# Kernel optimization log

Hardware: AMD Instinct MI355X
Metric: run time of the kernel (lower is better)

## Reference

```python
import jax, jax.numpy as jnp
import numpy as np
import math

D_MODEL = 1024
NUM_HEADS = 16
HEAD_DIM = D_MODEL // NUM_HEADS


def setup_inputs() -> dict:
    key = jax.random.key(0)
    ks = jax.random.split(key, 9)
    B, T = 4, 2048
    s = 1.0 / math.sqrt(D_MODEL)
    return {
        "x": jax.random.normal(ks[0], (B, T, D_MODEL), dtype=jnp.float32),
        "Wq": jax.random.normal(ks[1], (D_MODEL, D_MODEL), dtype=jnp.float32) * s,
        "bq": jnp.zeros((D_MODEL,), dtype=jnp.float32),
        "Wk": jax.random.normal(ks[2], (D_MODEL, D_MODEL), dtype=jnp.float32) * s,
        "bk": jnp.zeros((D_MODEL,), dtype=jnp.float32),
        "Wv": jax.random.normal(ks[3], (D_MODEL, D_MODEL), dtype=jnp.float32) * s,
        "bv": jnp.zeros((D_MODEL,), dtype=jnp.float32),
        "Wo": jax.random.normal(ks[4], (D_MODEL, D_MODEL), dtype=jnp.float32) * s,
        "bo": jnp.zeros((D_MODEL,), dtype=jnp.float32),
    }


def reference(x, Wq, bq, Wk, bk, Wv, bv, Wo, bo):
    # x: [B, T, D]. Weights stored as [in, out] (torch Linear weight transposed).
    B, T, D = x.shape
    H, Hd = NUM_HEADS, HEAD_DIM

    def heads(w, b):
        # [B,T,D] -> [B,H,T,Hd]
        return (x @ w + b).reshape(B, T, H, Hd).transpose(0, 2, 1, 3)

    q = heads(Wq, bq)
    k = heads(Wk, bk)
    v = heads(Wv, bv)

    scores = jnp.einsum("bhqd,bhkd->bhqk", q, k) / math.sqrt(Hd)
    attn = jax.nn.softmax(scores, axis=-1)  # dropout is identity in eval mode
    ctx = jnp.einsum("bhqk,bhkd->bhqd", attn, v)
    ctx = ctx.transpose(0, 2, 1, 3).reshape(B, T, D)
    return ctx @ Wo + bo
```

## Files before the change

kernel.cpp:

```cpp
#include <hip/hip_runtime.h>
#include <hip/hip_bf16.h>

#define D_MODEL 1024
#define NHEADS  16
#define HD      64
#define BATCH   4
#define SEQ     2048
#define MROWS   (BATCH*SEQ)

typedef __attribute__((ext_vector_type(8))) short bf16x8;
typedef __attribute__((ext_vector_type(4))) float f32x4;
typedef __attribute__((ext_vector_type(16))) float f32x16;
typedef __attribute__((ext_vector_type(2))) float f32x2;
typedef __attribute__((ext_vector_type(4))) unsigned int u32x4;
typedef __attribute__((ext_vector_type(2))) unsigned int u32x2;
#define MFMA16(a,b,c) __builtin_amdgcn_mfma_f32_16x16x32_bf16(a,b,c,0,0,0)
#define MFMA32(a,b,c) __builtin_amdgcn_mfma_f32_32x32x16_bf16(a,b,c,0,0,0)

__device__ __forceinline__ short f2bf(float f) {
    __hip_bfloat16 h = __float2bfloat16(f);
    return *reinterpret_cast<short*>(&h);
}
__device__ __forceinline__ unsigned cvtpk(float a, float b) {
    unsigned r; asm("v_cvt_pk_bf16_f32 %0, %1, %2" : "=v"(r) : "v"(a), "v"(b)); return r;
}
__device__ __forceinline__ float fexp2(float x) {
    float r; asm("v_exp_f32 %0, %1" : "=v"(r) : "v"(x)); return r;
}
__device__ __forceinline__ f32x2 pkadd(f32x2 a, f32x2 b) {
    f32x2 d; asm("v_pk_add_f32 %0, %1, %2" : "=v"(d) : "v"(a), "v"(b)); return d;
}
#define SH2(V,I) __builtin_shufflevector(V, V, I, (I)+1)

typedef const __attribute__((address_space(1))) unsigned char* gas_t;
typedef __attribute__((address_space(3))) unsigned char* las_t;
#define GLD16(gp, lp) __builtin_amdgcn_global_load_lds((gas_t)(gp), (las_t)(lp), 16, 0, 0)

__global__ __launch_bounds__(256) void prep(
    const float* __restrict__ x,
    const float* __restrict__ Wq, const float* __restrict__ Wk,
    const float* __restrict__ Wv, const float* __restrict__ Wo,
    short* __restrict__ xb,
    short* __restrict__ WqT, short* __restrict__ WkT,
    short* __restrict__ WvT, short* __restrict__ WoT)
{
    __shared__ float tile[64][65];
    const int bid = blockIdx.x;
    const int t = threadIdx.x;
    if (bid < 4096) {
        const size_t i = ((size_t)bid * 256 + t) * 8;
        float4 a = *reinterpret_cast<const float4*>(&x[i]);
        float4 b = *reinterpret_cast<const float4*>(&x[i + 4]);
        bf16x8 v;
        v[0]=f2bf(a.x); v[1]=f2bf(a.y); v[2]=f2bf(a.z); v[3]=f2bf(a.w);
        v[4]=f2bf(b.x); v[5]=f2bf(b.y); v[6]=f2bf(b.z); v[7]=f2bf(b.w);
        *reinterpret_cast<bf16x8*>(&xb[i]) = v;
        return;
    }
    const int tt = bid - 4096;
    const int w = tt >> 8;
    const int tl = tt & 255;
    const int bn = (tl & 15) * 64, bk = (tl >> 4) * 64;
    const float* W = (w==0)?Wq:(w==1)?Wk:(w==2)?Wv:Wo;
    short* out     = (w==0)?WqT:(w==1)?WkT:(w==2)?WvT:WoT;
    const int r = t >> 2, c0 = (t & 3) * 16;
    #pragma unroll
    for (int i = 0; i < 16; i += 4) {
        float4 v = *reinterpret_cast<const float4*>(&W[(size_t)(bk + r) * D_MODEL + bn + c0 + i]);
        tile[r][c0+i] = v.x; tile[r][c0+i+1] = v.y; tile[r][c0+i+2] = v.z; tile[r][c0+i+3] = v.w;
    }
    __syncthreads();
    bf16x8 H0, H1;
    #pragma unroll
    for (int i = 0; i < 8; i++) { H0[i] = f2bf(tile[c0 + i][r]); H1[i] = f2bf(tile[c0 + 8 + i][r]); }
    short* hp = &out[(size_t)(bn + r) * D_MODEL + bk + c0];
    *reinterpret_cast<bf16x8*>(hp) = H0;
    *reinterpret_cast<bf16x8*>(hp + 8) = H1;
}

__global__ __launch_bounds__(256) void gemm_qkv(
    const short* __restrict__ A,
    const short* __restrict__ WqT, const short* __restrict__ WkT, const short* __restrict__ WvT,
    const float* __restrict__ bq, const float* __restrict__ bk, const float* __restrict__ bv,
    short* __restrict__ qo, short* __restrict__ ko, short* __restrict__ vo,
    const float qscale)
{
    __shared__ short As[3][128 * 32];
    __shared__ short Bs[3][128 * 32];
    const int tid = threadIdx.x, wave = tid >> 6, lane = tid & 63;
    const int g = lane >> 4, li = lane & 15;
    const int lin = blockIdx.x + blockIdx.y * 24;
    const int swz = (lin & 7) * 192 + (lin >> 3);
    const int bx = swz % 24, by = swz / 24;
    const int which = bx >> 3;
    const int bm = by * 128, bn = (bx & 7) * 128;
    const int wr = wave >> 1, wc = wave & 1;
    const int lrow = lane >> 2, lcol = (lane & 3) * 8;

    const short* BT = (which == 0) ? WqT : (which == 1) ? WkT : WvT;
    const float* bias = (which == 0) ? bq : (which == 1) ? bk : bv;
    short* out = (which == 0) ? qo : (which == 1) ? ko : vo;
    const float scale = (which == 0) ? qscale : 1.0f;

    f32x4 acc[4][4];
    #pragma unroll
    for (int i = 0; i < 4; i++)
        #pragma unroll
        for (int j = 0; j < 4; j++)
            #pragma unroll
            for (int r = 0; r < 4; r++) acc[i][j][r] = 0.f;

#define STAGEG(KS, BUF) do { \
        const int k0_ = (KS) * 32; \
        _Pragma("unroll") \
        for (int c = 0; c < 2; c++) { \
            const int ch = wave + c * 4; \
            const int row = ch * 16 + lrow; \
            GLD16(&A [(size_t)(bm + row) * D_MODEL + k0_ + lcol], &As[BUF][ch * 512]); \
            GLD16(&BT[(size_t)(bn + row) * D_MODEL + k0_ + lcol], &Bs[BUF][ch * 512]); \
        } \
    } while (0)

    STAGEG(0, 0);
    STAGEG(1, 1);

    const int NSTEP = D_MODEL / 32;
    for (int ks = 0; ks < NSTEP; ks++) {
        const int cur = ks % 3;
        if (ks + 2 < NSTEP) {
            STAGEG(ks + 2, (ks + 2) % 3);
            asm volatile("s_waitcnt vmcnt(8)" ::: "memory");
        } else if (ks + 1 < NSTEP) {
            asm volatile("s_waitcnt vmcnt(4)" ::: "memory");
        } else {
            asm volatile("s_waitcnt vmcnt(0)" ::: "memory");
        }
        __builtin_amdgcn_s_barrier();
        __builtin_amdgcn_sched_barrier(0);

        bf16x8 af[4], bfr[4];
        #pragma unroll
        for (int mi = 0; mi < 4; mi++) af[mi]  = *reinterpret_cast<const bf16x8*>(&As[cur][(wr * 64 + mi * 16 + li) * 32 + g * 8]);
        #pragma unroll
        for (int ni = 0; ni < 4; ni++) bfr[ni] = *reinterpret_cast<const bf16x8*>(&Bs[cur][(wc * 64 + ni * 16 + li) * 32 + g * 8]);
        #pragma unroll
        for (int mi = 0; mi < 4; mi++)
            #pragma unroll
            for (int ni = 0; ni < 4; ni++)
                acc[mi][ni] = MFMA16(af[mi], bfr[ni], acc[mi][ni]);
        __builtin_amdgcn_s_barrier();
    }
#undef STAGEG

    #pragma unroll
    for (int mi = 0; mi < 4; mi++) {
        #pragma unroll
        for (int r = 0; r < 4; r++) {
            const int m = bm + wr * 64 + mi * 16 + g * 4 + r;
            const int b = m >> 11, t = m & (SEQ - 1);
            #pragma unroll
            for (int ni = 0; ni < 4; ni++) {
                const int n = bn + wc * 64 + ni * 16 + li;
                const float val = (acc[mi][ni][r] + bias[n]) * scale;
                const int h = n >> 6, hd = n & 63;
                if (which != 2) out[((size_t)((b * NHEADS + h) * SEQ + t)) * HD + hd] = f2bf(val);
                else            out[((size_t)((b * NHEADS + h) * HD + hd)) * SEQ + t] = f2bf(val);
            }
        }
    }
}

__global__ __launch_bounds__(256) void gemm_wo(
    const short* __restrict__ A, const short* __restrict__ BT,
    const float* __restrict__ bias, float* __restrict__ out)
{
    __shared__ short As[3][128 * 32];
    __shared__ short Bs[3][128 * 32];
    const int tid = threadIdx.x, wave = tid >> 6, lane = tid & 63;
    const int g = lane >> 4, li = lane & 15;
    const int lin = blockIdx.x + blockIdx.y * 8;
    const int swz = (lin & 7) * 64 + (lin >> 3);
    const int bm = (swz >> 3) * 128, bn = (swz & 7) * 128;
    const int wr = wave >> 1, wc = wave & 1;
    const int lrow = lane >> 2, lcol = (lane & 3) * 8;

    f32x4 acc[4][4];
    #pragma unroll
    for (int i = 0; i < 4; i++)
        #pragma unroll
        for (int j = 0; j < 4; j++)
            #pragma unroll
            for (int r = 0; r < 4; r++) acc[i][j][r] = 0.f;

#define STAGEG(KS, BUF) do { \
        const int k0_ = (KS) * 32; \
        _Pragma("unroll") \
        for (int c = 0; c < 2; c++) { \
            const int ch = wave + c * 4; \
            const int row = ch * 16 + lrow; \
            GLD16(&A [(size_t)(bm + row) * D_MODEL + k0_ + lcol], &As[BUF][ch * 512]); \
            GLD16(&BT[(size_t)(bn + row) * D_MODEL + k0_ + lcol], &Bs[BUF][ch * 512]); \
        } \
    } while (0)

    STAGEG(0, 0);
    STAGEG(1, 1);

    const int NSTEP = D_MODEL / 32;
    for (int ks = 0; ks < NSTEP; ks++) {
        const int cur = ks % 3;
        if (ks + 2 < NSTEP) {
            STAGEG(ks + 2, (ks + 2) % 3);
            asm volatile("s_waitcnt vmcnt(8)" ::: "memory");
        } else if (ks + 1 < NSTEP) {
            asm volatile("s_waitcnt vmcnt(4)" ::: "memory");
        } else {
            asm volatile("s_waitcnt vmcnt(0)" ::: "memory");
        }
        __builtin_amdgcn_s_barrier();
        __builtin_amdgcn_sched_barrier(0);

        bf16x8 af[4], bfr[4];
        #pragma unroll
        for (int mi = 0; mi < 4; mi++) af[mi]  = *reinterpret_cast<const bf16x8*>(&As[cur][(wr * 64 + mi * 16 + li) * 32 + g * 8]);
        #pragma unroll
        for (int ni = 0; ni < 4; ni++) bfr[ni] = *reinterpret_cast<const bf16x8*>(&Bs[cur][(wc * 64 + ni * 16 + li) * 32 + g * 8]);
        #pragma unroll
        for (int mi = 0; mi < 4; mi++)
            #pragma unroll
            for (int ni = 0; ni < 4; ni++)
                acc[mi][ni] = MFMA16(af[mi], bfr[ni], acc[mi][ni]);
        __builtin_amdgcn_s_barrier();
    }
#undef STAGEG

    #pragma unroll
    for (int mi = 0; mi < 4; mi++) {
        #pragma unroll
        for (int r = 0; r < 4; r++) {
            const int m = bm + wr * 64 + mi * 16 + g * 4 + r;
            #pragma unroll
            for (int ni = 0; ni < 4; ni++) {
                const int n = bn + wc * 64 + ni * 16 + li;
                out[(size_t)m * D_MODEL + n] = acc[mi][ni][r] + bias[n];
            }
        }
    }
}

__global__ __launch_bounds__(256) void attn_mfma(
    const short* __restrict__ q, const short* __restrict__ k,
    const short* __restrict__ vT, short* __restrict__ ch)
{
    __shared__ short Ks[3][64 * 64];
    __shared__ short Vs[3][64 * 64];

    const int bh = blockIdx.x;
    const int b  = bh >> 4, h = bh & (NHEADS - 1);
    const int qt = blockIdx.y;
    const int tid = threadIdx.x;
    const int wave = tid >> 6, lane = tid & 63;
    const int ql = lane & 31;
    const int hi = lane >> 5;
    const int lb = lane * 8;

    const short* qp = q + ((size_t)bh * SEQ + qt * 128 + wave * 32 + ql) * HD;
    const bf16x8 qf0 = *reinterpret_cast<const bf16x8*>(qp + 0  + hi * 8);
    const bf16x8 qf1 = *reinterpret_cast<const bf16x8*>(qp + 16 + hi * 8);
    const bf16x8 qf2 = *reinterpret_cast<const bf16x8*>(qp + 32 + hi * 8);
    const bf16x8 qf3 = *reinterpret_cast<const bf16x8*>(qp + 48 + hi * 8);

    f32x16 o0, o1, Z;
    #pragma unroll
    for (int i = 0; i < 16; i++) { o0[i] = 0.f; o1[i] = 0.f; Z[i] = 0.f; }
    float lR = 0.f;

    const short* kbase = k  + (size_t)bh * SEQ * HD;
    const short* vbase = vT + (size_t)bh * HD * SEQ;

    const int r0 = wave * 2, r1 = wave * 2 + 1;
    const int kof0 = ((r0 & 1) * 32 + ql) * HD + (r0 >> 1) * 16 + hi * 8;
    const int kof1 = ((r1 & 1) * 32 + ql) * HD + (r1 >> 1) * 16 + hi * 8;
    const size_t vof0 = (size_t)((r0 & 1) * 32 + ql) * SEQ + (r0 >> 1) * 16 + hi * 8;
    const size_t vof1 = (size_t)((r1 & 1) * 32 + ql) * SEQ + (r1 >> 1) * 16 + hi * 8;

#define STAGE(T, BUF) do { \
        const short* kg_ = kbase + (size_t)(T) * 64 * HD; \
        const short* vg_ = vbase + (size_t)(T) * 64; \
        GLD16(kg_ + kof0, &Ks[BUF][r0 * 512]); \
        GLD16(kg_ + kof1, &Ks[BUF][r1 * 512]); \
        GLD16(vg_ + vof0, &Vs[BUF][r0 * 512]); \
        GLD16(vg_ + vof1, &Vs[BUF][r1 * 512]); \
    } while (0)

    u32x4 pp[4];
    bf16x8 vr0[4], vr1[4];

    STAGE(0, 0);
    STAGE(1, 1);

    const int NT = SEQ / 64;
    for (int kt = 0; kt < NT; kt++) {
        if (kt + 1 < NT) asm volatile("s_waitcnt vmcnt(4)" ::: "memory");
        else             asm volatile("s_waitcnt vmcnt(0)" ::: "memory");
        __builtin_amdgcn_s_barrier();
        __builtin_amdgcn_sched_barrier(0);
        if (kt + 2 < NT) STAGE(kt + 2, (kt + 2) % 3);

        const short* Kb = Ks[kt % 3];
        const short* Vb = Vs[kt % 3];

        f32x16 s0, s1;
        __builtin_amdgcn_s_setprio(1);
#define QK_STEP(DC, QF, C0, C1) do { \
            const bf16x8 ka0 = *reinterpret_cast<const bf16x8*>(&Kb[((DC) * 2 + 0) * 512 + lb]); \
            const bf16x8 ka1 = *reinterpret_cast<const bf16x8*>(&Kb[((DC) * 2 + 1) * 512 + lb]); \
            s0 = MFMA32(ka0, QF, C0); \
            s1 = MFMA32(ka1, QF, C1); \
        } while (0)
        QK_STEP(0, qf0, Z, Z);
        QK_STEP(1, qf1, s0, s1);
        QK_STEP(2, qf2, s0, s1);
        QK_STEP(3, qf3, s0, s1);
#undef QK_STEP

        if (kt > 0) {
            #pragma unroll
            for (int KB = 0; KB < 4; KB++) {
                const bf16x8 pf = __builtin_bit_cast(bf16x8, pp[KB]);
                o0 = MFMA32(vr0[KB], pf, o0);
                o1 = MFMA32(vr1[KB], pf, o1);
            }
        }
        #pragma unroll
        for (int KB = 0; KB < 4; KB++) {
            vr0[KB] = *reinterpret_cast<const bf16x8*>(&Vb[(KB * 2 + 0) * 512 + lb]);
            vr1[KB] = *reinterpret_cast<const bf16x8*>(&Vb[(KB * 2 + 1) * 512 + lb]);
        }
        __builtin_amdgcn_s_setprio(0);

        #pragma unroll
        for (int i = 0; i < 16; i++) s0[i] = fexp2(s0[i]);
        #pragma unroll
        for (int i = 0; i < 16; i++) s1[i] = fexp2(s1[i]);
        {
            f32x2 p0 = pkadd(SH2(s0, 0), SH2(s0, 2));
            f32x2 p1 = pkadd(SH2(s0, 4), SH2(s0, 6));
            f32x2 p2 = pkadd(SH2(s0, 8), SH2(s0, 10));
            f32x2 p3 = pkadd(SH2(s0, 12), SH2(s0, 14));
            f32x2 p4 = pkadd(SH2(s1, 0), SH2(s1, 2));
            f32x2 p5 = pkadd(SH2(s1, 4), SH2(s1, 6));
            f32x2 p6 = pkadd(SH2(s1, 8), SH2(s1, 10));
            f32x2 p7 = pkadd(SH2(s1, 12), SH2(s1, 14));
            p0 = pkadd(p0, p1); p2 = pkadd(p2, p3);
            p4 = pkadd(p4, p5); p6 = pkadd(p6, p7);
            p0 = pkadd(p0, p2); p4 = pkadd(p4, p6);
            p0 = pkadd(p0, p4);
            float sum = p0[0] + p0[1];
            sum += __shfl_xor(sum, 32);
            lR += sum;
        }

#define PACK(KB, SS, B) do { \
            const unsigned a0 = cvtpk(SS[(B) + 0], SS[(B) + 1]); \
            const unsigned a1 = cvtpk(SS[(B) + 2], SS[(B) + 3]); \
            const unsigned a2 = cvtpk(SS[(B) + 4], SS[(B) + 5]); \
            const unsigned a3 = cvtpk(SS[(B) + 6], SS[(B) + 7]); \
            const u32x2 r02 = __builtin_amdgcn_permlane32_swap(a0, a2, false, false); \
            const u32x2 r13 = __builtin_amdgcn_permlane32_swap(a1, a3, false, false); \
            pp[KB][0] = r02[0]; pp[KB][1] = r13[0]; pp[KB][2] = r02[1]; pp[KB][3] = r13[1]; \
        } while (0)
        PACK(0, s0, 0); PACK(1, s0, 8); PACK(2, s1, 0); PACK(3, s1, 8);
#undef PACK

        asm volatile("s_waitcnt lgkmcnt(0)" ::: "memory");
        __builtin_amdgcn_sched_barrier(0);
    }
#undef STAGE

    #pragma unroll
    for (int KB = 0; KB < 4; KB++) {
        const bf16x8 pf = __builtin_bit_cast(bf16x8, pp[KB]);
        o0 = MFMA32(vr0[KB], pf, o0);
        o1 = MFMA32(vr1[KB], pf, o1);
    }

    const float inv = 1.0f / lR;
    const int t = qt * 128 + wave * 32 + ql;
    const size_t base = ((size_t)(b * SEQ + t)) * D_MODEL + h * HD;
    #pragma unroll
    for (int blk = 0; blk < 4; blk++) {
        uint2 w0, w1;
        w0.x = cvtpk(o0[4*blk + 0] * inv, o0[4*blk + 1] * inv);
        w0.y = cvtpk(o0[4*blk + 2] * inv, o0[4*blk + 3] * inv);
        w1.x = cvtpk(o1[4*blk + 0] * inv, o1[4*blk + 1] * inv);
        w1.y = cvtpk(o1[4*blk + 2] * inv, o1[4*blk + 3] * inv);
        *reinterpret_cast<uint2*>(&ch[base + 8*blk + 4*hi])      = w0;
        *reinterpret_cast<uint2*>(&ch[base + 32 + 8*blk + 4*hi]) = w1;
    }
}

extern "C" void kernel_launch(void* const* d_in, const int* in_sizes, int n_in,
                              void* d_out, int out_size, void* d_ws, size_t ws_size,
                              hipStream_t stream) {
    const float* x  = (const float*)d_in[0];
    const float* Wq = (const float*)d_in[1];
    const float* bq = (const float*)d_in[2];
    const float* Wk = (const float*)d_in[3];
    const float* bk = (const float*)d_in[4];
    const float* Wv = (const float*)d_in[5];
    const float* bv = (const float*)d_in[6];
    const float* Wo = (const float*)d_in[7];
    const float* bo = (const float*)d_in[8];

    const size_t S1 = (size_t)MROWS * D_MODEL;
    const size_t SW = (size_t)D_MODEL * D_MODEL;
    short* xb  = (short*)d_ws;
    short* qb  = xb + S1;
    short* kb  = qb + S1;
    short* vb  = kb + S1;
    short* chb = vb + S1;
    short* WqT = chb + S1;
    short* WkT = WqT + SW;
    short* WvT = WkT + SW;
    short* WoT = WvT + SW;

    prep<<<5120, 256, 0, stream>>>(x, Wq, Wk, Wv, Wo, xb, WqT, WkT, WvT, WoT);

    const float QSCALE = 0.125f * 1.4426950408889634f;
    gemm_qkv<<<dim3(24, 64), 256, 0, stream>>>(xb, WqT, WkT, WvT, bq, bk, bv,
                                               qb, kb, vb, QSCALE);
    attn_mfma<<<dim3(BATCH * NHEADS, SEQ / 128), 256, 0, stream>>>(qb, kb, vb, chb);
    gemm_wo<<<dim3(8, 64), 256, 0, stream>>>(chb, WoT, bo, (float*)d_out);
}
```

Before: 232.0 us.

## Store K/V in pre-blocked tile layout and issue prefetch before barrier

The QKV projection epilogue now writes K and V directly in a per-64-row tile, MFMA-fragment-ordered layout. The attention kernel can then stage each K/V tile with fully contiguous 16-byte loads instead of strided gathers, which for V^T meant striding by SEQ. The prefetch of tile kt+2 is also moved ahead of the wait and barrier, with a deeper vmcnt and an extra end-of-iteration barrier to protect buffer reuse. This trades scattered stores in the projection epilogue and one more barrier per iteration for better load coalescing and earlier overlap of loads.

```diff
diff --git a/kernel.cpp b/kernel.cpp
--- a/kernel.cpp
+++ b/kernel.cpp
@@ -7,6 +7,7 @@
 #define BATCH   4
 #define SEQ     2048
 #define MROWS   (BATCH*SEQ)
+#define NKV     (SEQ/64)
 
 typedef __attribute__((ext_vector_type(8))) short bf16x8;
 typedef __attribute__((ext_vector_type(4))) float f32x4;
@@ -163,8 +164,21 @@
                 const int n = bn + wc * 64 + ni * 16 + li;
                 const float val = (acc[mi][ni][r] + bias[n]) * scale;
                 const int h = n >> 6, hd = n & 63;
-                if (which != 2) out[((size_t)((b * NHEADS + h) * SEQ + t)) * HD + hd] = f2bf(val);
-                else            out[((size_t)((b * NHEADS + h) * HD + hd)) * SEQ + t] = f2bf(val);
+                const int bh = b * NHEADS + h;
+                const short sv = f2bf(val);
+                if (which == 0) {
+                    out[((size_t)bh * SEQ + t) * HD + hd] = sv;
+                } else if (which == 1) {
+                    const int kt = t >> 6, trow = t & 63;
+                    const int rh = trow >> 5, rl = trow & 31;
+                    const int dc = hd >> 4, hh = (hd >> 3) & 1, j = hd & 7;
+                    out[((((size_t)bh * NKV + kt) * 8 + dc * 2 + rh) * 64 + hh * 32 + rl) * 8 + j] = sv;
+                } else {
+                    const int kt = t >> 6, trow = t & 63;
+                    const int kb2 = trow >> 4, hh = (trow >> 3) & 1, j = trow & 7;
+                    const int vh = hd >> 5, rl = hd & 31;
+                    out[((((size_t)bh * NKV + kt) * 8 + kb2 * 2 + vh) * 64 + hh * 32 + rl) * 8 + j] = sv;
+                }
             }
         }
     }
@@ -249,8 +263,8 @@
 }
 
 __global__ __launch_bounds__(256) void attn_mfma(
-    const short* __restrict__ q, const short* __restrict__ k,
-    const short* __restrict__ vT, short* __restrict__ ch)
+    const short* __restrict__ q, const short* __restrict__ kblk,
+    const short* __restrict__ vblk, short* __restrict__ ch)
 {
     __shared__ short Ks[3][64 * 64];
     __shared__ short Vs[3][64 * 64];
@@ -275,22 +289,15 @@
     for (int i = 0; i < 16; i++) { o0[i] = 0.f; o1[i] = 0.f; Z[i] = 0.f; }
     float lR = 0.f;
 
-    const short* kbase = k  + (size_t)bh * SEQ * HD;
-    const short* vbase = vT + (size_t)bh * HD * SEQ;
-
     const int r0 = wave * 2, r1 = wave * 2 + 1;
-    const int kof0 = ((r0 & 1) * 32 + ql) * HD + (r0 >> 1) * 16 + hi * 8;
-    const int kof1 = ((r1 & 1) * 32 + ql) * HD + (r1 >> 1) * 16 + hi * 8;
-    const size_t vof0 = (size_t)((r0 & 1) * 32 + ql) * SEQ + (r0 >> 1) * 16 + hi * 8;
-    const size_t vof1 = (size_t)((r1 & 1) * 32 + ql) * SEQ + (r1 >> 1) * 16 + hi * 8;
 
 #define STAGE(T, BUF) do { \
-        const short* kg_ = kbase + (size_t)(T) * 64 * HD; \
-        const short* vg_ = vbase + (size_t)(T) * 64; \
-        GLD16(kg_ + kof0, &Ks[BUF][r0 * 512]); \
-        GLD16(kg_ + kof1, &Ks[BUF][r1 * 512]); \
-        GLD16(vg_ + vof0, &Vs[BUF][r0 * 512]); \
-        GLD16(vg_ + vof1, &Vs[BUF][r1 * 512]); \
+        const short* kg_ = kblk + ((size_t)(bh * NKV + (T)) * 8) * 512; \
+        const short* vg_ = vblk + ((size_t)(bh * NKV + (T)) * 8) * 512; \
+        GLD16(kg_ + r0 * 512 + lb, &Ks[BUF][r0 * 512]); \
+        GLD16(kg_ + r1 * 512 + lb, &Ks[BUF][r1 * 512]); \
+        GLD16(vg_ + r0 * 512 + lb, &Vs[BUF][r0 * 512]); \
+        GLD16(vg_ + r1 * 512 + lb, &Vs[BUF][r1 * 512]); \
     } while (0)
 
     u32x4 pp[4];
@@ -299,13 +306,18 @@
     STAGE(0, 0);
     STAGE(1, 1);
 
-    const int NT = SEQ / 64;
+    const int NT = NKV;
     for (int kt = 0; kt < NT; kt++) {
-        if (kt + 1 < NT) asm volatile("s_waitcnt vmcnt(4)" ::: "memory");
-        else             asm volatile("s_waitcnt vmcnt(0)" ::: "memory");
+        if (kt + 2 < NT) {
+            STAGE(kt + 2, (kt + 2) % 3);
+            asm volatile("s_waitcnt vmcnt(8)" ::: "memory");
+        } else if (kt + 1 < NT) {
+            asm volatile("s_waitcnt vmcnt(4)" ::: "memory");
+        } else {
+            asm volatile("s_waitcnt vmcnt(0)" ::: "memory");
+        }
         __builtin_amdgcn_s_barrier();
         __builtin_amdgcn_sched_barrier(0);
-        if (kt + 2 < NT) STAGE(kt + 2, (kt + 2) % 3);
 
         const short* Kb = Ks[kt % 3];
         const short* Vb = Vs[kt % 3];
@@ -375,6 +387,7 @@
 
         asm volatile("s_waitcnt lgkmcnt(0)" ::: "memory");
         __builtin_amdgcn_sched_barrier(0);
+        __builtin_amdgcn_s_barrier();
     }
 #undef STAGE
 
```

Measured after the change: 199.8 us. 13.9% less time.
